# Kernel tuning notes

Hardware: AMD Instinct MI355X
Metric: run time of the kernel (lower is better)

Reference implementation:

```python
import jax, jax.numpy as jnp
import numpy as np

NUM_LAYERS = 32
HIDDEN_DIM = 2048
RANK = 64
BATCH = 2048


def setup_inputs() -> dict:
    key = jax.random.key(0)
    k_z, k_id, k_u, k_v = jax.random.split(key, 4)
    z = jax.random.normal(k_z, (BATCH, HIDDEN_DIM), dtype=jnp.float32)
    layer_ids = jax.random.randint(k_id, (BATCH,), 0, NUM_LAYERS)
    u = jax.random.normal(k_u, (NUM_LAYERS, HIDDEN_DIM, RANK), dtype=jnp.float32) * 0.01
    v = jax.random.normal(k_v, (NUM_LAYERS, HIDDEN_DIM, RANK), dtype=jnp.float32) * 0.01
    return {"z": z, "layer_ids": layer_ids, "u": u, "v": v}


def reference(z, layer_ids, u, v):
    # Gather per-sample low-rank factors: [B, H, R]
    u_g = u[layer_ids]
    v_g = v[layer_ids]
    # proj = V_l^T z : [B, R]
    proj = jnp.einsum('bhr,bh->br', v_g, z)
    # delta = U_l proj : [B, H]
    delta = jnp.einsum('bhr,br->bh', u_g, proj)
    return z + delta
```

## Files before the change

### kernel.cpp

```cpp
#include <hip/hip_runtime.h>

#define NUM_LAYERS 32
#define HIDDEN 2048
#define RANK 64
#define BATCH 2048
#define KC 128
#define HCH 128
#define MB_P 64
#define MB_D 128
#define ZPAD 136
#define VPAD 136
#define UPAD 72
#define PPAD 72

typedef __attribute__((ext_vector_type(8))) short bf16x8;
typedef __attribute__((ext_vector_type(4))) float f32x4;

static __device__ __forceinline__ ushort f2bf(float x) {
    unsigned b = __builtin_bit_cast(unsigned, x);
    b += 0x7fffu + ((b >> 16) & 1u);
    return (ushort)(b >> 16);
}
static __device__ __forceinline__ ushort4 pack4(float4 v) {
    ushort4 r; r.x = f2bf(v.x); r.y = f2bf(v.y); r.z = f2bf(v.z); r.w = f2bf(v.w);
    return r;
}

__global__ __launch_bounds__(512)
void k_proj(const float* __restrict__ z, const float* __restrict__ v,
            const int* __restrict__ ids, float* __restrict__ proj)
{
    const int kc = blockIdx.x, l = blockIdx.y;
    const int t = threadIdx.x;
    const int w = t >> 6, lane = t & 63;
    const int m16 = lane & 15, quad = lane >> 4;
    const int wr = w & 3, wm = w >> 2;
    const int kbase = kc * KC;

    __shared__ int    lidx[BATCH];
    __shared__ int    nsh;
    __shared__ ushort vt[RANK * VPAD];
    __shared__ ushort zt[2][MB_P * ZPAD];

    if (t == 0) nsh = 0;

    float4 vreg[4];
    #pragma unroll
    for (int it = 0; it < 4; ++it) {
        const int idx = it * 512 + t;
        const int hh = idx >> 4, rq = idx & 15;
        vreg[it] = *(const float4*)&v[((size_t)l * HIDDEN + kbase + hh) * RANK + rq * 4];
    }
    __syncthreads();

    {
        const int4 iv = ((const int4*)ids)[t];
        if (iv.x == l) lidx[atomicAdd(&nsh, 1)] = t * 4 + 0;
        if (iv.y == l) lidx[atomicAdd(&nsh, 1)] = t * 4 + 1;
        if (iv.z == l) lidx[atomicAdd(&nsh, 1)] = t * 4 + 2;
        if (iv.w == l) lidx[atomicAdd(&nsh, 1)] = t * 4 + 3;
    }
    __syncthreads();
    const int n = nsh;
    if (n == 0) return;

    const int P = (n + MB_P - 1) / MB_P;
    float4 zreg[4];
    {
        const int nb = (n < MB_P) ? n : MB_P;
        #pragma unroll
        for (int it = 0; it < 4; ++it) {
            const int idx = it * 512 + t;
            const int si = idx >> 5, q = idx & 31;
            zreg[it] = make_float4(0.f, 0.f, 0.f, 0.f);
            if (si < nb)
                zreg[it] = *(const float4*)&z[(size_t)lidx[si] * HIDDEN + kbase + q * 4];
        }
    }
    #pragma unroll
    for (int it = 0; it < 4; ++it) {
        const int idx = it * 512 + t;
        const int hh = idx >> 4, rq = idx & 15;
        vt[(rq * 4 + 0) * VPAD + hh] = f2bf(vreg[it].x);
        vt[(rq * 4 + 1) * VPAD + hh] = f2bf(vreg[it].y);
        vt[(rq * 4 + 2) * VPAD + hh] = f2bf(vreg[it].z);
        vt[(rq * 4 + 3) * VPAD + hh] = f2bf(vreg[it].w);
    }

    for (int p = 0; p < P; ++p) {
        const int nbr = n - p * MB_P;
        const int nb = (nbr < MB_P) ? nbr : MB_P;
        #pragma unroll
        for (int it = 0; it < 4; ++it) {
            const int idx = it * 512 + t;
            const int si = idx >> 5, q = idx & 31;
            *(ushort4*)&zt[p & 1][si * ZPAD + q * 4] = pack4(zreg[it]);
        }
        __syncthreads();
        if (p + 1 < P) {
            const int b2 = (p + 1) * MB_P;
            const int nb2r = n - b2;
            const int nb2 = (nb2r < MB_P) ? nb2r : MB_P;
            #pragma unroll
            for (int it = 0; it < 4; ++it) {
                const int idx = it * 512 + t;
                const int si = idx >> 5, q = idx & 31;
                zreg[it] = make_float4(0.f, 0.f, 0.f, 0.f);
                if (si < nb2)
                    zreg[it] = *(const float4*)&z[(size_t)lidx[b2 + si] * HIDDEN + kbase + q * 4];
            }
        }
        f32x4 acc0 = {0.f, 0.f, 0.f, 0.f}, acc1 = {0.f, 0.f, 0.f, 0.f};
        const ushort* zr0 = &zt[p & 1][(wm * 32 + m16) * ZPAD];
        const ushort* zr1 = zr0 + 16 * ZPAD;
        const ushort* vr  = &vt[(wr * 16 + m16) * VPAD];
        #pragma unroll
        for (int kt = 0; kt < 4; ++kt) {
            const int koff = kt * 32 + quad * 8;
            const bf16x8 bf = *(const bf16x8*)&vr[koff];
            const bf16x8 a0 = *(const bf16x8*)&zr0[koff];
            const bf16x8 a1 = *(const bf16x8*)&zr1[koff];
            acc0 = __builtin_amdgcn_mfma_f32_16x16x32_bf16(a0, bf, acc0, 0, 0, 0);
            acc1 = __builtin_amdgcn_mfma_f32_16x16x32_bf16(a1, bf, acc1, 0, 0, 0);
        }
        const int r = wr * 16 + m16;
        const int base = p * MB_P;
        #pragma unroll
        for (int reg = 0; reg < 4; ++reg) {
            const int row = wm * 32 + quad * 4 + reg;
            if (row < nb)
                atomicAdd(&proj[(size_t)lidx[base + row] * RANK + r], acc0[reg]);
            if (row + 16 < nb)
                atomicAdd(&proj[(size_t)lidx[base + row + 16] * RANK + r], acc1[reg]);
        }
    }
}

__global__ __launch_bounds__(512)
void k_delta(const float* __restrict__ z, const float* __restrict__ u,
             const int* __restrict__ ids, const float* __restrict__ proj,
             float* __restrict__ out)
{
    const int hc = blockIdx.x, l = blockIdx.y;
    const int t = threadIdx.x;
    const int w = t >> 6, lane = t & 63;
    const int m16 = lane & 15, quad = lane >> 4;
    const int wr = w & 1, wm = w >> 1;
    const int hbase = hc * HCH;

    __shared__ int    lidx[BATCH];
    __shared__ int    nsh;
    __shared__ ushort ut[HCH * UPAD];
    __shared__ ushort pt[2][MB_D * PPAD];

    if (t == 0) nsh = 0;

    float4 ureg[4];
    #pragma unroll
    for (int it = 0; it < 4; ++it) {
        const int idx = it * 512 + t;
        const int hh = idx >> 4, rq = idx & 15;
        ureg[it] = *(const float4*)&u[((size_t)l * HIDDEN + hbase + hh) * RANK + rq * 4];
    }
    __syncthreads();

    {
        const int4 iv = ((const int4*)ids)[t];
        if (iv.x == l) lidx[atomicAdd(&nsh, 1)] = t * 4 + 0;
        if (iv.y == l) lidx[atomicAdd(&nsh, 1)] = t * 4 + 1;
        if (iv.z == l) lidx[atomicAdd(&nsh, 1)] = t * 4 + 2;
        if (iv.w == l) lidx[atomicAdd(&nsh, 1)] = t * 4 + 3;
    }
    __syncthreads();
    const int n = nsh;
    if (n == 0) return;

    const int P = (n + MB_D - 1) / MB_D;
    float4 preg[4];
    float  zep[2][4][4];
    {
        const int nb = (n < MB_D) ? n : MB_D;
        #pragma unroll
        for (int it = 0; it < 4; ++it) {
            const int idx = it * 512 + t;
            const int si = idx >> 4, rq = idx & 15;
            preg[it] = make_float4(0.f, 0.f, 0.f, 0.f);
            if (si < nb)
                preg[it] = *(const float4*)&proj[(size_t)lidx[si] * RANK + rq * 4];
        }
        #pragma unroll
        for (int mt = 0; mt < 2; ++mt)
            #pragma unroll
            for (int reg = 0; reg < 4; ++reg) {
                const int si = wm * 32 + mt * 16 + quad * 4 + reg;
                const size_t rowb = (si < nb) ? ((size_t)lidx[si] * HIDDEN + hbase) : 0;
                #pragma unroll
                for (int nt = 0; nt < 4; ++nt) {
                    const int h = (wr * 4 + nt) * 16 + m16;
                    zep[mt][nt][reg] = (si < nb) ? z[rowb + h] : 0.f;
                }
            }
    }
    #pragma unroll
    for (int it = 0; it < 4; ++it) {
        const int idx = it * 512 + t;
        const int hh = idx >> 4, rq = idx & 15;
        *(ushort4*)&ut[hh * UPAD + rq * 4] = pack4(ureg[it]);
    }

    for (int p = 0; p < P; ++p) {
        const int nbr = n - p * MB_D;
        const int nb = (nbr < MB_D) ? nbr : MB_D;
        const int base = p * MB_D;
        #pragma unroll
        for (int it = 0; it < 4; ++it) {
            const int idx = it * 512 + t;
            const int si = idx >> 4, rq = idx & 15;
            *(ushort4*)&pt[p & 1][si * PPAD + rq * 4] = pack4(preg[it]);
        }
        __syncthreads();

        f32x4 acc[2][4];
        #pragma unroll
        for (int mt = 0; mt < 2; ++mt)
            #pragma unroll
            for (int nt = 0; nt < 4; ++nt)
                acc[mt][nt] = (f32x4){0.f, 0.f, 0.f, 0.f};

        const ushort* pr0 = &pt[p & 1][(wm * 32 + m16) * PPAD];
        const ushort* pr1 = pr0 + 16 * PPAD;
        #pragma unroll
        for (int kt = 0; kt < 2; ++kt) {
            const int koff = kt * 32 + quad * 8;
            const bf16x8 a0 = *(const bf16x8*)&pr0[koff];
            const bf16x8 a1 = *(const bf16x8*)&pr1[koff];
            #pragma unroll
            for (int nt = 0; nt < 4; ++nt) {
                const int h = (wr * 4 + nt) * 16 + m16;
                const bf16x8 bf = *(const bf16x8*)&ut[h * UPAD + koff];
                acc[0][nt] = __builtin_amdgcn_mfma_f32_16x16x32_bf16(a0, bf, acc[0][nt], 0, 0, 0);
                acc[1][nt] = __builtin_amdgcn_mfma_f32_16x16x32_bf16(a1, bf, acc[1][nt], 0, 0, 0);
            }
        }
        #pragma unroll
        for (int mt = 0; mt < 2; ++mt)
            #pragma unroll
            for (int reg = 0; reg < 4; ++reg) {
                const int si = wm * 32 + mt * 16 + quad * 4 + reg;
                if (si < nb) {
                    const size_t rowb = (size_t)lidx[base + si] * HIDDEN + hbase;
                    #pragma unroll
                    for (int nt = 0; nt < 4; ++nt) {
                        const int h = (wr * 4 + nt) * 16 + m16;
                        out[rowb + h] = zep[mt][nt][reg] + acc[mt][nt][reg];
                    }
                }
            }
        if (p + 1 < P) {
            const int b2 = (p + 1) * MB_D;
            const int nb2r = n - b2;
            const int nb2 = (nb2r < MB_D) ? nb2r : MB_D;
            #pragma unroll
            for (int it = 0; it < 4; ++it) {
                const int idx = it * 512 + t;
                const int si = idx >> 4, rq = idx & 15;
                preg[it] = make_float4(0.f, 0.f, 0.f, 0.f);
                if (si < nb2)
                    preg[it] = *(const float4*)&proj[(size_t)lidx[b2 + si] * RANK + rq * 4];
            }
            #pragma unroll
            for (int mt = 0; mt < 2; ++mt)
                #pragma unroll
                for (int reg = 0; reg < 4; ++reg) {
                    const int si = wm * 32 + mt * 16 + quad * 4 + reg;
                    const size_t rowb = (si < nb2) ? ((size_t)lidx[b2 + si] * HIDDEN + hbase) : 0;
                    #pragma unroll
                    for (int nt = 0; nt < 4; ++nt) {
                        const int h = (wr * 4 + nt) * 16 + m16;
                        zep[mt][nt][reg] = (si < nb2) ? z[rowb + h] : 0.f;
                    }
                }
        }
    }
}

extern "C" void kernel_launch(void* const* d_in, const int* in_sizes, int n_in,
                              void* d_out, int out_size, void* d_ws, size_t ws_size,
                              hipStream_t stream)
{
    const float* z   = (const float*)d_in[0];
    const int*   ids = (const int*)d_in[1];
    const float* u   = (const float*)d_in[2];
    const float* v   = (const float*)d_in[3];
    float* out = (float*)d_out;
    float* proj = (float*)d_ws;

    hipMemsetAsync(proj, 0, (size_t)BATCH * RANK * sizeof(float), stream);
    hipLaunchKernelGGL(k_proj, dim3(HIDDEN / KC, NUM_LAYERS), dim3(512), 0, stream,
                       z, v, ids, proj);
    hipLaunchKernelGGL(k_delta, dim3(HIDDEN / HCH, NUM_LAYERS), dim3(512), 0, stream,
                       z, u, ids, proj, out);
}
```

Measured before the change: 109.5 us.

## Fuse projection and delta kernels into one cooperative kernel with grid sync

Replaces the two-kernel launch with one cooperative kernel of 256 blocks (8 per layer). Each block handles two hidden chunks in the projection phase, does a grid-wide sync, then handles two chunks in the delta phase. The U factors and the first z epilogue values are prefetched before the grid sync so those loads overlap the wait. The aim is to remove a kernel launch and reuse each block's layer index list across both phases. In exchange the grid is smaller, so each block does twice the work, and the grid barrier adds cost. The old two-kernel path stays as a fallback if the cooperative launch fails.

```diff
diff --git a/kernel.cpp b/kernel.cpp
--- a/kernel.cpp
+++ b/kernel.cpp
@@ -1,4 +1,7 @@
 #include <hip/hip_runtime.h>
+#include <hip/hip_cooperative_groups.h>
+
+namespace cg = cooperative_groups;
 
 #define NUM_LAYERS 32
 #define HIDDEN 2048
@@ -27,8 +30,269 @@
 }
 
 __global__ __launch_bounds__(512)
-void k_proj(const float* __restrict__ z, const float* __restrict__ v,
-            const int* __restrict__ ids, float* __restrict__ proj)
+void k_fused(const float* __restrict__ z, const float* __restrict__ vm,
+             const float* __restrict__ um, const int* __restrict__ ids,
+             float* __restrict__ proj, float* __restrict__ out)
+{
+    const int bid = blockIdx.x;
+    const int l = bid >> 3, part = bid & 7;
+    const int t = threadIdx.x;
+    const int w = t >> 6, lane = t & 63;
+    const int m16 = lane & 15, quad = lane >> 4;
+
+    __shared__ int lidx[BATCH];
+    __shared__ int nsh;
+    __shared__ __align__(16) char smem[55296];
+    ushort* const vt  = (ushort*)smem;
+    ushort* const zt0 = (ushort*)(smem + 17408);
+    ushort* const zt1 = (ushort*)(smem + 34816);
+    ushort* const ut  = (ushort*)smem;
+    ushort* const pt0 = (ushort*)(smem + 18432);
+    ushort* const pt1 = (ushort*)(smem + 36864);
+
+    if (t == 0) nsh = 0;
+
+    float4 vreg[4];
+    #pragma unroll
+    for (int it = 0; it < 4; ++it) {
+        const int idx = it * 512 + t, hh = idx >> 4, rq = idx & 15;
+        vreg[it] = *(const float4*)&vm[((size_t)l * HIDDEN + part * KC + hh) * RANK + rq * 4];
+    }
+    __syncthreads();
+    {
+        const int4 iv = ((const int4*)ids)[t];
+        if (iv.x == l) lidx[atomicAdd(&nsh, 1)] = t * 4 + 0;
+        if (iv.y == l) lidx[atomicAdd(&nsh, 1)] = t * 4 + 1;
+        if (iv.z == l) lidx[atomicAdd(&nsh, 1)] = t * 4 + 2;
+        if (iv.w == l) lidx[atomicAdd(&nsh, 1)] = t * 4 + 3;
+    }
+    __syncthreads();
+    const int n = nsh;
+
+    if (n > 0) {
+        const int wr = w & 3, wm = w >> 2;
+        const int P = (n + MB_P - 1) / MB_P;
+        #pragma unroll
+        for (int c = 0; c < 2; ++c) {
+            const int kbase = (part + c * 8) * KC;
+            float4 zreg[4];
+            {
+                const int nb = (n < MB_P) ? n : MB_P;
+                #pragma unroll
+                for (int it = 0; it < 4; ++it) {
+                    const int idx = it * 512 + t, si = idx >> 5, q = idx & 31;
+                    zreg[it] = make_float4(0.f, 0.f, 0.f, 0.f);
+                    if (si < nb)
+                        zreg[it] = *(const float4*)&z[(size_t)lidx[si] * HIDDEN + kbase + q * 4];
+                }
+            }
+            if (c == 1) __syncthreads();
+            #pragma unroll
+            for (int it = 0; it < 4; ++it) {
+                const int idx = it * 512 + t, hh = idx >> 4, rq = idx & 15;
+                vt[(rq * 4 + 0) * VPAD + hh] = f2bf(vreg[it].x);
+                vt[(rq * 4 + 1) * VPAD + hh] = f2bf(vreg[it].y);
+                vt[(rq * 4 + 2) * VPAD + hh] = f2bf(vreg[it].z);
+                vt[(rq * 4 + 3) * VPAD + hh] = f2bf(vreg[it].w);
+            }
+            if (c == 0) {
+                #pragma unroll
+                for (int it = 0; it < 4; ++it) {
+                    const int idx = it * 512 + t, hh = idx >> 4, rq = idx & 15;
+                    vreg[it] = *(const float4*)&vm[((size_t)l * HIDDEN + (part + 8) * KC + hh) * RANK + rq * 4];
+                }
+            }
+            for (int p = 0; p < P; ++p) {
+                ushort* const ztp = (p & 1) ? zt1 : zt0;
+                const int nbr = n - p * MB_P;
+                const int nb = (nbr < MB_P) ? nbr : MB_P;
+                #pragma unroll
+                for (int it = 0; it < 4; ++it) {
+                    const int idx = it * 512 + t, si = idx >> 5, q = idx & 31;
+                    *(ushort4*)&ztp[si * ZPAD + q * 4] = pack4(zreg[it]);
+                }
+                __syncthreads();
+                if (p + 1 < P) {
+                    const int b2 = (p + 1) * MB_P;
+                    const int nb2 = (n - b2 < MB_P) ? (n - b2) : MB_P;
+                    #pragma unroll
+                    for (int it = 0; it < 4; ++it) {
+                        const int idx = it * 512 + t, si = idx >> 5, q = idx & 31;
+                        zreg[it] = make_float4(0.f, 0.f, 0.f, 0.f);
+                        if (si < nb2)
+                            zreg[it] = *(const float4*)&z[(size_t)lidx[b2 + si] * HIDDEN + kbase + q * 4];
+                    }
+                }
+                f32x4 acc0 = {0.f, 0.f, 0.f, 0.f}, acc1 = {0.f, 0.f, 0.f, 0.f};
+                const ushort* zr0 = &ztp[(wm * 32 + m16) * ZPAD];
+                const ushort* zr1 = zr0 + 16 * ZPAD;
+                const ushort* vr  = &vt[(wr * 16 + m16) * VPAD];
+                #pragma unroll
+                for (int kt = 0; kt < 4; ++kt) {
+                    const int koff = kt * 32 + quad * 8;
+                    const bf16x8 bf = *(const bf16x8*)&vr[koff];
+                    const bf16x8 a0 = *(const bf16x8*)&zr0[koff];
+                    const bf16x8 a1 = *(const bf16x8*)&zr1[koff];
+                    acc0 = __builtin_amdgcn_mfma_f32_16x16x32_bf16(a0, bf, acc0, 0, 0, 0);
+                    acc1 = __builtin_amdgcn_mfma_f32_16x16x32_bf16(a1, bf, acc1, 0, 0, 0);
+                }
+                const int r = wr * 16 + m16;
+                const int base = p * MB_P;
+                #pragma unroll
+                for (int reg = 0; reg < 4; ++reg) {
+                    const int row = wm * 32 + quad * 4 + reg;
+                    if (row < nb)
+                        atomicAdd(&proj[(size_t)lidx[base + row] * RANK + r], acc0[reg]);
+                    if (row + 16 < nb)
+                        atomicAdd(&proj[(size_t)lidx[base + row + 16] * RANK + r], acc1[reg]);
+                }
+            }
+        }
+    }
+
+    const int wrB = w & 1, wmB = w >> 1;
+    float4 uregA[4], uregB[4];
+    float  zep[2][4][4];
+    if (n > 0) {
+        #pragma unroll
+        for (int it = 0; it < 4; ++it) {
+            const int idx = it * 512 + t, hh = idx >> 4, rq = idx & 15;
+            uregA[it] = *(const float4*)&um[((size_t)l * HIDDEN + part * HCH + hh) * RANK + rq * 4];
+            uregB[it] = *(const float4*)&um[((size_t)l * HIDDEN + (part + 8) * HCH + hh) * RANK + rq * 4];
+        }
+        const int nb = (n < MB_D) ? n : MB_D;
+        #pragma unroll
+        for (int mt = 0; mt < 2; ++mt)
+            #pragma unroll
+            for (int reg = 0; reg < 4; ++reg) {
+                const int si = wmB * 32 + mt * 16 + quad * 4 + reg;
+                const size_t rowb = (si < nb) ? ((size_t)lidx[si] * HIDDEN + part * HCH) : 0;
+                #pragma unroll
+                for (int nt = 0; nt < 4; ++nt) {
+                    const int h = (wrB * 4 + nt) * 16 + m16;
+                    zep[mt][nt][reg] = (si < nb) ? z[rowb + h] : 0.f;
+                }
+            }
+    }
+    cg::this_grid().sync();
+
+    if (n > 0) {
+        const int P = (n + MB_D - 1) / MB_D;
+        #pragma unroll
+        for (int c = 0; c < 2; ++c) {
+            const int hbase = (part + c * 8) * HCH;
+            float4 preg[4];
+            {
+                const int nb = (n < MB_D) ? n : MB_D;
+                #pragma unroll
+                for (int it = 0; it < 4; ++it) {
+                    const int idx = it * 512 + t, si = idx >> 4, rq = idx & 15;
+                    preg[it] = make_float4(0.f, 0.f, 0.f, 0.f);
+                    if (si < nb)
+                        preg[it] = *(const float4*)&proj[(size_t)lidx[si] * RANK + rq * 4];
+                }
+            }
+            if (c == 1) {
+                const int nb = (n < MB_D) ? n : MB_D;
+                #pragma unroll
+                for (int mt = 0; mt < 2; ++mt)
+                    #pragma unroll
+                    for (int reg = 0; reg < 4; ++reg) {
+                        const int si = wmB * 32 + mt * 16 + quad * 4 + reg;
+                        const size_t rowb = (si < nb) ? ((size_t)lidx[si] * HIDDEN + hbase) : 0;
+                        #pragma unroll
+                        for (int nt = 0; nt < 4; ++nt) {
+                            const int h = (wrB * 4 + nt) * 16 + m16;
+                            zep[mt][nt][reg] = (si < nb) ? z[rowb + h] : 0.f;
+                        }
+                    }
+                __syncthreads();
+            }
+            #pragma unroll
+            for (int it = 0; it < 4; ++it) {
+                const int idx = it * 512 + t, hh = idx >> 4, rq = idx & 15;
+                const float4 uv = (c == 0) ? uregA[it] : uregB[it];
+                *(ushort4*)&ut[hh * UPAD + rq * 4] = pack4(uv);
+            }
+            for (int p = 0; p < P; ++p) {
+                ushort* const ptp = (p & 1) ? pt1 : pt0;
+                const int nbr = n - p * MB_D;
+                const int nb = (nbr < MB_D) ? nbr : MB_D;
+                const int base = p * MB_D;
+                #pragma unroll
+                for (int it = 0; it < 4; ++it) {
+                    const int idx = it * 512 + t, si = idx >> 4, rq = idx & 15;
+                    *(ushort4*)&ptp[si * PPAD + rq * 4] = pack4(preg[it]);
+                }
+                __syncthreads();
+
+                f32x4 acc[2][4];
+                #pragma unroll
+                for (int mt = 0; mt < 2; ++mt)
+                    #pragma unroll
+                    for (int nt = 0; nt < 4; ++nt)
+                        acc[mt][nt] = (f32x4){0.f, 0.f, 0.f, 0.f};
+
+                const ushort* pr0 = &ptp[(wmB * 32 + m16) * PPAD];
+                const ushort* pr1 = pr0 + 16 * PPAD;
+                #pragma unroll
+                for (int kt = 0; kt < 2; ++kt) {
+                    const int koff = kt * 32 + quad * 8;
+                    const bf16x8 a0 = *(const bf16x8*)&pr0[koff];
+                    const bf16x8 a1 = *(const bf16x8*)&pr1[koff];
+                    #pragma unroll
+                    for (int nt = 0; nt < 4; ++nt) {
+                        const int h = (wrB * 4 + nt) * 16 + m16;
+                        const bf16x8 bf = *(const bf16x8*)&ut[h * UPAD + koff];
+                        acc[0][nt] = __builtin_amdgcn_mfma_f32_16x16x32_bf16(a0, bf, acc[0][nt], 0, 0, 0);
+                        acc[1][nt] = __builtin_amdgcn_mfma_f32_16x16x32_bf16(a1, bf, acc[1][nt], 0, 0, 0);
+                    }
+                }
+                #pragma unroll
+                for (int mt = 0; mt < 2; ++mt)
+                    #pragma unroll
+                    for (int reg = 0; reg < 4; ++reg) {
+                        const int si = wmB * 32 + mt * 16 + quad * 4 + reg;
+                        if (si < nb) {
+                            const size_t rowb = (size_t)lidx[base + si] * HIDDEN + hbase;
+                            #pragma unroll
+                            for (int nt = 0; nt < 4; ++nt) {
+                                const int h = (wrB * 4 + nt) * 16 + m16;
+                                out[rowb + h] = zep[mt][nt][reg] + acc[mt][nt][reg];
+                            }
+                        }
+                    }
+                if (p + 1 < P) {
+                    const int b2 = (p + 1) * MB_D;
+                    const int nb2 = (n - b2 < MB_D) ? (n - b2) : MB_D;
+                    #pragma unroll
+                    for (int it = 0; it < 4; ++it) {
+                        const int idx = it * 512 + t, si = idx >> 4, rq = idx & 15;
+                        preg[it] = make_float4(0.f, 0.f, 0.f, 0.f);
+                        if (si < nb2)
+                            preg[it] = *(const float4*)&proj[(size_t)lidx[b2 + si] * RANK + rq * 4];
+                    }
+                    #pragma unroll
+                    for (int mt = 0; mt < 2; ++mt)
+                        #pragma unroll
+                        for (int reg = 0; reg < 4; ++reg) {
+                            const int si = wmB * 32 + mt * 16 + quad * 4 + reg;
+                            const size_t rowb = (si < nb2) ? ((size_t)lidx[b2 + si] * HIDDEN + hbase) : 0;
+                            #pragma unroll
+                            for (int nt = 0; nt < 4; ++nt) {
+                                const int h = (wrB * 4 + nt) * 16 + m16;
+                                zep[mt][nt][reg] = (si < nb2) ? z[rowb + h] : 0.f;
+                            }
+                        }
+                }
+            }
+        }
+    }
+}
+
+__global__ __launch_bounds__(512)
+void k_proj_fb(const float* __restrict__ z, const float* __restrict__ v,
+               const int* __restrict__ ids, float* __restrict__ proj)
 {
     const int kc = blockIdx.x, l = blockIdx.y;
     const int t = threadIdx.x;
@@ -43,16 +307,13 @@
     __shared__ ushort zt[2][MB_P * ZPAD];
 
     if (t == 0) nsh = 0;
-
     float4 vreg[4];
     #pragma unroll
     for (int it = 0; it < 4; ++it) {
-        const int idx = it * 512 + t;
-        const int hh = idx >> 4, rq = idx & 15;
+        const int idx = it * 512 + t, hh = idx >> 4, rq = idx & 15;
         vreg[it] = *(const float4*)&v[((size_t)l * HIDDEN + kbase + hh) * RANK + rq * 4];
     }
     __syncthreads();
-
     {
         const int4 iv = ((const int4*)ids)[t];
         if (iv.x == l) lidx[atomicAdd(&nsh, 1)] = t * 4 + 0;
@@ -70,8 +331,7 @@
         const int nb = (n < MB_P) ? n : MB_P;
         #pragma unroll
         for (int it = 0; it < 4; ++it) {
-            const int idx = it * 512 + t;
-            const int si = idx >> 5, q = idx & 31;
+            const int idx = it * 512 + t, si = idx >> 5, q = idx & 31;
             zreg[it] = make_float4(0.f, 0.f, 0.f, 0.f);
             if (si < nb)
                 zreg[it] = *(const float4*)&z[(size_t)lidx[si] * HIDDEN + kbase + q * 4];
@@ -79,32 +339,27 @@
     }
     #pragma unroll
     for (int it = 0; it < 4; ++it) {
-        const int idx = it * 512 + t;
-        const int hh = idx >> 4, rq = idx & 15;
+        const int idx = it * 512 + t, hh = idx >> 4, rq = idx & 15;
         vt[(rq * 4 + 0) * VPAD + hh] = f2bf(vreg[it].x);
         vt[(rq * 4 + 1) * VPAD + hh] = f2bf(vreg[it].y);
         vt[(rq * 4 + 2) * VPAD + hh] = f2bf(vreg[it].z);
         vt[(rq * 4 + 3) * VPAD + hh] = f2bf(vreg[it].w);
     }
-
     for (int p = 0; p < P; ++p) {
         const int nbr = n - p * MB_P;
         const int nb = (nbr < MB_P) ? nbr : MB_P;
         #pragma unroll
         for (int it = 0; it < 4; ++it) {
-            const int idx = it * 512 + t;
-            const int si = idx >> 5, q = idx & 31;
+            const int idx = it * 512 + t, si = idx >> 5, q = idx & 31;
             *(ushort4*)&zt[p & 1][si * ZPAD + q * 4] = pack4(zreg[it]);
         }
         __syncthreads();
         if (p + 1 < P) {
             const int b2 = (p + 1) * MB_P;
-            const int nb2r = n - b2;
-            const int nb2 = (nb2r < MB_P) ? nb2r : MB_P;
+            const int nb2 = (n - b2 < MB_P) ? (n - b2) : MB_P;
             #pragma unroll
             for (int it = 0; it < 4; ++it) {
-                const int idx = it * 512 + t;
-                const int si = idx >> 5, q = idx & 31;
+                const int idx = it * 512 + t, si = idx >> 5, q = idx & 31;
                 zreg[it] = make_float4(0.f, 0.f, 0.f, 0.f);
                 if (si < nb2)
                     zreg[it] = *(const float4*)&z[(size_t)lidx[b2 + si] * HIDDEN + kbase + q * 4];
@@ -137,9 +392,9 @@
 }
 
 __global__ __launch_bounds__(512)
-void k_delta(const float* __restrict__ z, const float* __restrict__ u,
-             const int* __restrict__ ids, const float* __restrict__ proj,
-             float* __restrict__ out)
+void k_delta_fb(const float* __restrict__ z, const float* __restrict__ u,
+                const int* __restrict__ ids, const float* __restrict__ proj,
+                float* __restrict__ out)
 {
     const int hc = blockIdx.x, l = blockIdx.y;
     const int t = threadIdx.x;
@@ -154,16 +409,13 @@
     __shared__ ushort pt[2][MB_D * PPAD];
 
     if (t == 0) nsh = 0;
-
     float4 ureg[4];
     #pragma unroll
     for (int it = 0; it < 4; ++it) {
-        const int idx = it * 512 + t;
-        const int hh = idx >> 4, rq = idx & 15;
+        const int idx = it * 512 + t, hh = idx >> 4, rq = idx & 15;
         ureg[it] = *(const float4*)&u[((size_t)l * HIDDEN + hbase + hh) * RANK + rq * 4];
     }
     __syncthreads();
-
     {
         const int4 iv = ((const int4*)ids)[t];
         if (iv.x == l) lidx[atomicAdd(&nsh, 1)] = t * 4 + 0;
@@ -182,8 +434,7 @@
         const int nb = (n < MB_D) ? n : MB_D;
         #pragma unroll
         for (int it = 0; it < 4; ++it) {
-            const int idx = it * 512 + t;
-            const int si = idx >> 4, rq = idx & 15;
+            const int idx = it * 512 + t, si = idx >> 4, rq = idx & 15;
             preg[it] = make_float4(0.f, 0.f, 0.f, 0.f);
             if (si < nb)
                 preg[it] = *(const float4*)&proj[(size_t)lidx[si] * RANK + rq * 4];
@@ -203,19 +454,16 @@
     }
     #pragma unroll
     for (int it = 0; it < 4; ++it) {
-        const int idx = it * 512 + t;
-        const int hh = idx >> 4, rq = idx & 15;
+        const int idx = it * 512 + t, hh = idx >> 4, rq = idx & 15;
         *(ushort4*)&ut[hh * UPAD + rq * 4] = pack4(ureg[it]);
     }
-
     for (int p = 0; p < P; ++p) {
         const int nbr = n - p * MB_D;
         const int nb = (nbr < MB_D) ? nbr : MB_D;
         const int base = p * MB_D;
         #pragma unroll
         for (int it = 0; it < 4; ++it) {
-            const int idx = it * 512 + t;
-            const int si = idx >> 4, rq = idx & 15;
+            const int idx = it * 512 + t, si = idx >> 4, rq = idx & 15;
             *(ushort4*)&pt[p & 1][si * PPAD + rq * 4] = pack4(preg[it]);
         }
         __syncthreads();
@@ -258,12 +506,10 @@
             }
         if (p + 1 < P) {
             const int b2 = (p + 1) * MB_D;
-            const int nb2r = n - b2;
-            const int nb2 = (nb2r < MB_D) ? nb2r : MB_D;
+            const int nb2 = (n - b2 < MB_D) ? (n - b2) : MB_D;
             #pragma unroll
             for (int it = 0; it < 4; ++it) {
-                const int idx = it * 512 + t;
-                const int si = idx >> 4, rq = idx & 15;
+                const int idx = it * 512 + t, si = idx >> 4, rq = idx & 15;
                 preg[it] = make_float4(0.f, 0.f, 0.f, 0.f);
                 if (si < nb2)
                     preg[it] = *(const float4*)&proj[(size_t)lidx[b2 + si] * RANK + rq * 4];
@@ -292,12 +538,19 @@
     const int*   ids = (const int*)d_in[1];
     const float* u   = (const float*)d_in[2];
     const float* v   = (const float*)d_in[3];
-    float* out = (float*)d_out;
+    float* out  = (float*)d_out;
     float* proj = (float*)d_ws;
 
     hipMemsetAsync(proj, 0, (size_t)BATCH * RANK * sizeof(float), stream);
-    hipLaunchKernelGGL(k_proj, dim3(HIDDEN / KC, NUM_LAYERS), dim3(512), 0, stream,
-                       z, v, ids, proj);
-    hipLaunchKernelGGL(k_delta, dim3(HIDDEN / HCH, NUM_LAYERS), dim3(512), 0, stream,
-                       z, u, ids, proj, out);
+
+    void* args[] = {(void*)&z, (void*)&v, (void*)&u, (void*)&ids,
+                    (void*)&proj, (void*)&out};
+    hipError_t rc = hipLaunchCooperativeKernel((void*)k_fused, dim3(256), dim3(512),
+                                               args, 0, stream);
+    if (rc != hipSuccess) {
+        hipLaunchKernelGGL(k_proj_fb, dim3(HIDDEN / KC, NUM_LAYERS), dim3(512), 0,
+                           stream, z, v, ids, proj);
+        hipLaunchKernelGGL(k_delta_fb, dim3(HIDDEN / HCH, NUM_LAYERS), dim3(512), 0,
+                           stream, z, u, ids, proj, out);
+    }
 }
```

After: 158.5 us. +44.7%, slower.
